# Kernel tuning notes

Measured on AMD Instinct MI355X. Metric: run time of the kernel, lower is better.

Reference implementation:

```python
import jax, jax.numpy as jnp
import numpy as np

B, DIM, NX, NY = 4, 64, 256, 256
HEADS, DIM_HEAD, LATENT, DIM_OUT, KM = 4, 32, 128, 64, 2
DH = DIM_HEAD * KM  # LowRankKernel head dim (also RoPE dim) = 64
EPS = 1e-5
MIN_FREQ = 1.0 / 64.0  # RotaryEmbedding default in FactFormer/LNS repo


def _gelu(x):
    return jax.nn.gelu(x, approximate=False)  # torch nn.GELU default (erf)


def _conv1x1(u, w):
    # u: [b,c,h,w], w: [out,c]  (1x1 conv == channel matmul)
    return jnp.einsum('bchw,oc->bohw', u, w)


def _pooling_reducer(x, win, ln_g, ln_b, w1, w2, b2):
    # x: [b, n_keep, n_pool, c] -> Linear, mean-pool over n_pool, LN+FFN
    h = jnp.einsum('bnmc,hc->bnmh', x, win).mean(axis=2)  # [b, n, hid]
    m = h.mean(axis=-1, keepdims=True)
    v = h.var(axis=-1, keepdims=True)
    h = (h - m) / jnp.sqrt(v + EPS) * ln_g + ln_b
    return _gelu(h @ w1.T) @ w2.T + b2  # [b, n, latent]


def _rope_freqs(n):
    pos = jnp.linspace(0.0, 1.0, n) / MIN_FREQ  # scale/min_freq = 64
    inv = 1.0 / (10000.0 ** (jnp.arange(0, DH, 2, dtype=jnp.float32) / DH))
    f = pos[:, None] * inv[None, :]            # [n, DH//2]
    return jnp.concatenate([f, f], axis=-1)    # [n, DH]


def _apply_rope(x, f):
    # rotate_half = cat(-x2, x1) on half-split (FactFormer convention)
    d = x.shape[-1] // 2
    rot = jnp.concatenate([-x[..., d:], x[..., :d]], axis=-1)
    return x * jnp.cos(f) + rot * jnp.sin(f)


def _low_rank_kernel(x, wqk):
    # x: [b, n, latent] -> K: [b, heads, n, n]; scaling=1, dropout=Identity, qk_norm=False
    b, n, _ = x.shape
    qk = x @ wqk.T
    q, k = jnp.split(qk, 2, axis=-1)
    q = q.reshape(b, n, HEADS, DH).transpose(0, 2, 1, 3)
    k = k.reshape(b, n, HEADS, DH).transpose(0, 2, 1, 3)
    f = _rope_freqs(n)
    q = _apply_rope(q, f)
    k = _apply_rope(k, f)
    return jnp.einsum('bhid,bhjd->bhij', q, k)


def _forward(u, gn_w, gn_b, w_in_proj, w_to_in,
             px_win, px_ln_g, px_ln_b, px_w1, px_w2, px_b2,
             py_win, py_ln_g, py_ln_b, py_w1, py_w2, py_b2,
             kx_wqk, ky_wqk, out_w1, out_w2):
    # GroupNorm(1, dim): normalize over (C,H,W) per sample, affine
    m = u.mean(axis=(1, 2, 3), keepdims=True)
    v = u.var(axis=(1, 2, 3), keepdims=True)
    un = (u - m) / jnp.sqrt(v + EPS) * gn_w[None, :, None, None] + gn_b[None, :, None, None]
    u_phi = _conv1x1(un, w_in_proj)  # [b, heads*dim_head, nx, ny]
    ui = _conv1x1(un, w_to_in)       # [b, dim, nx, ny]
    # to_x: pool over ny -> tokens along nx; to_y: pool over nx -> tokens along ny
    ux = _pooling_reducer(ui.transpose(0, 2, 3, 1), px_win, px_ln_g, px_ln_b, px_w1, px_w2, px_b2)  # [b, nx, latent]
    uy = _pooling_reducer(ui.transpose(0, 3, 2, 1), py_win, py_ln_g, py_ln_b, py_w1, py_w2, py_b2)  # [b, ny, latent]
    kx = _low_rank_kernel(ux, kx_wqk)  # [b, h, nx, nx]
    ky = _low_rank_kernel(uy, ky_wqk)  # [b, h, ny, ny]
    b, hc, nx, ny = u_phi.shape
    up = u_phi.reshape(b, HEADS, hc // HEADS, nx, ny)
    up = jnp.einsum('bhij,bhcjm->bhcim', kx, up)
    up = jnp.einsum('bhlm,bhcim->bhcil', ky, up)
    up = up.reshape(b, hc, nx, ny)
    # InstanceNorm2d (no affine, no running stats)
    m2 = up.mean(axis=(2, 3), keepdims=True)
    v2 = up.var(axis=(2, 3), keepdims=True)
    upn = (up - m2) / jnp.sqrt(v2 + EPS)
    out = _conv1x1(_gelu(_conv1x1(upn, out_w1)), out_w2)
    return out + u


def setup_inputs() -> dict:
    key = jax.random.key(0)
    ks = jax.random.split(key, 16)
    def w(k, shape, s=0.02):
        return (jax.random.normal(k, shape) * s).astype(jnp.float32)
    return {
        'u': jax.random.normal(ks[0], (B, DIM, NX, NY), dtype=jnp.float32),
        'gn_w': jnp.ones((DIM,), jnp.float32), 'gn_b': jnp.zeros((DIM,), jnp.float32),
        'w_in_proj': w(ks[1], (HEADS * DIM_HEAD, DIM)),
        'w_to_in': w(ks[2], (DIM, DIM)),
        'px_win': w(ks[3], (DIM, DIM)),
        'px_ln_g': jnp.ones((DIM,), jnp.float32), 'px_ln_b': jnp.zeros((DIM,), jnp.float32),
        'px_w1': w(ks[4], (2 * DIM, DIM)), 'px_w2': w(ks[5], (LATENT, 2 * DIM)),
        'px_b2': jnp.zeros((LATENT,), jnp.float32),
        'py_win': w(ks[6], (DIM, DIM)),
        'py_ln_g': jnp.ones((DIM,), jnp.float32), 'py_ln_b': jnp.zeros((DIM,), jnp.float32),
        'py_w1': w(ks[7], (2 * DIM, DIM)), 'py_w2': w(ks[8], (LATENT, 2 * DIM)),
        'py_b2': jnp.zeros((LATENT,), jnp.float32),
        'kx_wqk': w(ks[9], (2 * HEADS * DH, LATENT)),
        'ky_wqk': w(ks[10], (2 * HEADS * DH, LATENT)),
        'out_w1': w(ks[11], (DIM_OUT, HEADS * DIM_HEAD)),
        'out_w2': w(ks[12], (DIM_OUT, DIM_OUT)),
    }


def reference(u, gn_w, gn_b, w_in_proj, w_to_in,
              px_win, px_ln_g, px_ln_b, px_w1, px_w2, px_b2,
              py_win, py_ln_g, py_ln_b, py_w1, py_w2, py_b2,
              kx_wqk, ky_wqk, out_w1, out_w2):
    return _forward(u, gn_w, gn_b, w_in_proj, w_to_in,
                    px_win, px_ln_g, px_ln_b, px_w1, px_w2, px_b2,
                    py_win, py_ln_g, py_ln_b, py_w1, py_w2, py_b2,
                    kx_wqk, ky_wqk, out_w1, out_w2)
```

## Files before the change

kernel.cpp:

```cpp
#include <hip/hip_runtime.h>
#include <math.h>

typedef unsigned short ushort_t;
typedef unsigned int uint_t;
typedef __attribute__((ext_vector_type(8))) short s8v;
typedef __attribute__((ext_vector_type(4))) float f4;

#define NPIX 65536
#define EPS_ 1e-5f

__device__ __forceinline__ float bf2f(ushort_t u){ return __uint_as_float(((uint_t)u)<<16); }
__device__ __forceinline__ ushort_t f2bf(float f){
  uint_t u = __float_as_uint(f);
  uint_t r = (u + 0x7fffu + ((u>>16)&1u)) >> 16;
  return (ushort_t)r;
}
__device__ __forceinline__ float bflo(uint_t p){ return __uint_as_float(p<<16); }
__device__ __forceinline__ float bfhi(uint_t p){ return __uint_as_float(p & 0xffff0000u); }
__device__ __forceinline__ uint_t packbf(float a, float b){ return (uint_t)f2bf(a) | ((uint_t)f2bf(b)<<16); }

__device__ __forceinline__ f4 MFMA(s8v a, s8v b, f4 c){
  return __builtin_amdgcn_mfma_f32_16x16x32_bf16(a, b, c, 0, 0, 0);
}

__device__ __forceinline__ float wave_sum(float v){
  #pragma unroll
  for(int m=32;m>=1;m>>=1) v += __shfl_xor(v, m, 64);
  return v;
}

__global__ __launch_bounds__(256) void k1_stats(const float* __restrict__ u,
    float* __restrict__ part, float* __restrict__ pc, float* __restrict__ poolx){
  int blk = blockIdx.x; int b = blk>>8; int c = (blk>>2)&63; int iq = blk&3;
  int t = threadIdx.x; int lane = t&63; int w = t>>6;
  const float* up = u + ((size_t)(b*64+c))*NPIX + iq*64*256;
  __shared__ float sCol[4][256];
  __shared__ float red[8];
  float4 cs4 = {0.f,0.f,0.f,0.f};
  float ss = 0.f;
  #pragma unroll 4
  for(int r16=0;r16<16;r16++){
    int r = w*16 + r16;
    float4 v = *(const float4*)(up + r*256 + lane*4);
    cs4.x+=v.x; cs4.y+=v.y; cs4.z+=v.z; cs4.w+=v.w;
    ss += v.x*v.x+v.y*v.y+v.z*v.z+v.w*v.w;
    float rs = wave_sum(v.x+v.y+v.z+v.w);
    if(lane==0) poolx[(b*256 + iq*64 + r)*64 + c] = rs*(1.f/256.f);
  }
  *(float4*)&sCol[w][lane*4] = cs4;
  float ssw = wave_sum(ss);
  if(lane==0) red[w] = ssw;
  __syncthreads();
  float colsum = sCol[0][t]+sCol[1][t]+sCol[2][t]+sCol[3][t];
  pc[((b*64+c)*4+iq)*256 + t] = colsum;
  float s1 = wave_sum(colsum);
  if(lane==0) red[4+w] = s1;
  __syncthreads();
  if(t==0){
    part[((b*64+c)*4+iq)*2]   = red[4]+red[5]+red[6]+red[7];
    part[((b*64+c)*4+iq)*2+1] = red[0]+red[1]+red[2]+red[3];
  }
}

__global__ void k2_fin(const float* __restrict__ part, float* __restrict__ gnmv){
  int t = threadIdx.x; int b = t>>6; int i = t&63;
  float S1=0.f, S2=0.f;
  #pragma unroll
  for(int q=0;q<4;q++){
    S1 += part[((b*64+i)*4+q)*2];
    S2 += part[((b*64+i)*4+q)*2+1];
  }
  S1 = wave_sum(S1); S2 = wave_sum(S2);
  if(i==0){
    const float inv = 1.f/4194304.f;
    float m = S1*inv; float v = S2*inv - m*m;
    gnmv[b*2] = m; gnmv[b*2+1] = rsqrtf(v + EPS_);
  }
}

__global__ __launch_bounds__(256) void k8a_fold(const float* __restrict__ gnmv,
    const float* __restrict__ gnw, const float* __restrict__ gnb,
    const float* __restrict__ w_in_proj, const float* __restrict__ out_w2,
    ushort_t* __restrict__ wpb, float* __restrict__ c0g, ushort_t* __restrict__ w2b){
  int b = blockIdx.x; int t = threadIdx.x;
  __shared__ float scs[64], shs[64];
  if(t<64){
    float mean = gnmv[b*2], rstd = gnmv[b*2+1];
    float sc = rstd*gnw[t];
    scs[t] = sc; shs[t] = gnb[t] - mean*sc;
  }
  __syncthreads();
  int oc = t>>1, h = t&1;
  float c0 = 0.f;
  for(int k=0;k<32;k++){
    int ch = h*32 + k;
    float wv = w_in_proj[oc*64 + ch];
    wpb[((size_t)b*128 + oc)*64 + ch] = f2bf(wv*scs[ch]);
    c0 += wv*shs[ch];
  }
  c0 += __shfl_xor(c0, 1, 64);
  if(h==0) c0g[b*128 + oc] = c0;
  if(b==0){
    for(int e=t;e<4096;e+=256) w2b[e] = f2bf(out_w2[e]);
  }
}

__global__ void k8b_fold(const float* __restrict__ istat,
    const float* __restrict__ out_w1, ushort_t* __restrict__ W1b,
    float* __restrict__ bias1){
  int b = blockIdx.x; int t = threadIdx.x;
  __shared__ float ms[128], rss[128];
  ms[t] = istat[(b*128+t)*2];       rss[t] = istat[(b*128+t)*2+1];
  ms[64+t] = istat[(b*128+64+t)*2]; rss[64+t] = istat[(b*128+64+t)*2+1];
  __syncthreads();
  float bias = 0.f;
  for(int ch=0;ch<128;ch++){
    float wv = out_w1[t*128 + ch];
    float wr = wv*rss[ch];
    W1b[((size_t)b*64 + t)*128 + ch] = f2bf(wr);
    bias += wr*ms[ch];
  }
  bias1[b*64 + t] = bias;
}

__global__ __launch_bounds__(128) void k3_reduce(
    const float* __restrict__ poolx, const float* __restrict__ pc,
    const float* __restrict__ gnmv,
    const float* __restrict__ gnw, const float* __restrict__ gnb,
    const float* __restrict__ w_to_in,
    const float* __restrict__ xwin, const float* __restrict__ xlg, const float* __restrict__ xlb,
    const float* __restrict__ xw1, const float* __restrict__ xw2, const float* __restrict__ xb2,
    const float* __restrict__ ywin, const float* __restrict__ ylg, const float* __restrict__ ylb,
    const float* __restrict__ yw1, const float* __restrict__ yw2, const float* __restrict__ yb2,
    float* __restrict__ ux, float* __restrict__ uy){
  int id = blockIdx.x;
  int side = id >> 10; int r = id & 1023; int b = r>>8; int i = r&255;
  const float* win = side ? ywin : xwin;
  const float* lg  = side ? ylg  : xlg;
  const float* lb  = side ? ylb  : xlb;
  const float* w1  = side ? yw1  : xw1;
  const float* w2  = side ? yw2  : xw2;
  const float* b2  = side ? yb2  : xb2;
  float* outp = side ? uy : ux;
  int t = threadIdx.x;
  __shared__ float pn[64], t1[64], hh[64], f1[128];
  float mean = gnmv[b*2], rstd = gnmv[b*2+1];
  if(t<64){
    float pv;
    if(side){
      const float* p = pc + ((size_t)(b*64+t)*4)*256 + i;
      pv = (p[0] + p[256] + p[512] + p[768]) * (1.f/256.f);
    } else {
      pv = poolx[(b*256+i)*64 + t];
    }
    pn[t] = (pv - mean)*rstd*gnw[t] + gnb[t];
  }
  __syncthreads();
  if(t<64){
    float acc=0.f; const float* wr = w_to_in + t*64;
    #pragma unroll 8
    for(int c=0;c<64;c++) acc += pn[c]*wr[c];
    t1[t]=acc;
  }
  __syncthreads();
  if(t<64){
    float acc=0.f; const float* wr = win + t*64;
    #pragma unroll 8
    for(int c=0;c<64;c++) acc += t1[c]*wr[c];
    hh[t]=acc;
  }
  __syncthreads();
  if(t<64){
    float v = hh[t];
    float s = wave_sum(v);
    float ss = wave_sum(v*v);
    float m2 = s*(1.f/64.f);
    float var = ss*(1.f/64.f) - m2*m2;
    float rs2 = rsqrtf(var + EPS_);
    hh[t] = (v - m2)*rs2*lg[t] + lb[t];
  }
  __syncthreads();
  {
    float acc=0.f; const float* wr = w1 + t*64;
    #pragma unroll 8
    for(int c=0;c<64;c++) acc += hh[c]*wr[c];
    f1[t] = 0.5f*acc*(1.f + erff(acc*0.70710678118654752f));
  }
  __syncthreads();
  {
    float acc=0.f; const float* wr = w2 + t*128;
    #pragma unroll 8
    for(int j=0;j<128;j++) acc += f1[j]*wr[j];
    outp[(b*256+i)*128 + t] = acc + b2[t];
  }
}

__global__ __launch_bounds__(256) void k4_gemm(
    const float* __restrict__ ux, const float* __restrict__ uy,
    const float* __restrict__ wqkx, const float* __restrict__ wqky,
    ushort_t* __restrict__ qxb, ushort_t* __restrict__ kxTb,
    ushort_t* __restrict__ qyb, ushort_t* __restrict__ kyTb){
  int blk = blockIdx.x;
  int nt = blk&3; int mt = (blk>>2)&1; int b = (blk>>3)&3; int side = blk>>5;
  const float* x  = (side? uy:ux) + (size_t)(b*256 + mt*128)*128;
  const float* wq = (side? wqky:wqkx) + (size_t)nt*128*128;
  ushort_t* qb  = side? qyb : qxb;
  ushort_t* kTb = side? kyTb : kxTb;

  __shared__ __align__(16) ushort_t sA[128*136];
  __shared__ __align__(16) ushort_t sB[128*136];

  int t = threadIdx.x; int lane = t&63; int w = t>>6; int lr = lane&15; int lg = lane>>4;
  for(int e=t;e<4096;e+=256){
    int row = e>>5, c4 = (e&31)*4;
    float4 v = *(const float4*)(x + row*128 + c4);
    uint2 pk; pk.x = packbf(v.x,v.y); pk.y = packbf(v.z,v.w);
    *(uint2*)&sA[row*136 + c4] = pk;
    float4 wv = *(const float4*)(wq + row*128 + c4);
    uint2 wk; wk.x = packbf(wv.x,wv.y); wk.y = packbf(wv.z,wv.w);
    *(uint2*)&sB[row*136 + c4] = wk;
  }
  __syncthreads();
  const f4 fz = {0.f,0.f,0.f,0.f};
  f4 acc[2][8];
  #pragma unroll
  for(int it=0;it<2;it++)
    #pragma unroll
    for(int n2=0;n2<8;n2++) acc[it][n2]=fz;
  #pragma unroll
  for(int kc=0;kc<4;kc++){
    s8v bf[8];
    #pragma unroll
    for(int n2=0;n2<8;n2++)
      bf[n2] = *(const s8v*)&sB[(n2*16+lr)*136 + kc*32 + lg*8];
    #pragma unroll
    for(int it=0;it<2;it++){
      s8v a = *(const s8v*)&sA[(w*32+it*16+lr)*136 + kc*32 + lg*8];
      #pragma unroll
      for(int n2=0;n2<8;n2++)
        acc[it][n2] = MFMA(a, bf[n2], acc[it][n2]);
    }
  }
  if(nt < 2){
    #pragma unroll
    for(int it=0;it<2;it++){
      #pragma unroll
      for(int n2=0;n2<8;n2++){
        int o = nt*128 + n2*16 + lr;
        int h = o>>6, dd = o&63, t32 = dd&31;
        float invf = expf(-(float)t32*(9.210340371976184f/32.f));
        size_t base = (size_t)(b*4+h)*16384;
        #pragma unroll
        for(int r=0;r<4;r++){
          int i = mt*128 + w*32 + it*16 + lg*4 + r;
          float f = (64.f/255.f)*(float)i*invf;
          float sn, cs; __sincosf(f, &sn, &cs);
          float pair = acc[it][n2^2][r];
          float rot = ((n2&2)==0)? -pair : pair;
          float v = acc[it][n2][r]*cs + rot*sn;
          qb[base + (size_t)i*64 + dd] = f2bf(v);
        }
      }
    }
  } else {
    __syncthreads();
    #pragma unroll
    for(int it=0;it<2;it++){
      #pragma unroll
      for(int n2=0;n2<8;n2++){
        int ol = n2*16 + lr;
        int o = nt*128 + ol;
        int t32 = o&31;
        float invf = expf(-(float)t32*(9.210340371976184f/32.f));
        #pragma unroll
        for(int r=0;r<4;r++){
          int il = w*32 + it*16 + lg*4 + r;
          int i = mt*128 + il;
          float f = (64.f/255.f)*(float)i*invf;
          float sn, cs; __sincosf(f, &sn, &cs);
          float pair = acc[it][n2^2][r];
          float rot = ((n2&2)==0)? -pair : pair;
          float v = acc[it][n2][r]*cs + rot*sn;
          sA[ol*136 + il] = f2bf(v);
        }
      }
    }
    __syncthreads();
    {
      int row = t>>1, half = t&1;
      int h = (nt-2)*2 + (row>>6), dd = row&63;
      ushort_t* dst = kTb + (size_t)(b*4+h)*16384 + (size_t)dd*256 + mt*128 + half*64;
      const ushort_t* src = &sA[row*136 + half*64];
      #pragma unroll
      for(int j=0;j<8;j++)
        *(uint4*)(dst + j*8) = *(const uint4*)(src + j*8);
    }
  }
}

__global__ __launch_bounds__(256) void k5s_sums(const ushort_t* __restrict__ kxTb,
    const ushort_t* __restrict__ kyTb, float* __restrict__ ksum){
  int bh = blockIdx.x; int t = threadIdx.x;
  int row = t>>2, g = t&3;
  const ushort_t* kx = kxTb + (size_t)bh*16384 + row*256 + g*64;
  float s = 0.f;
  #pragma unroll
  for(int j=0;j<8;j++){
    uint4 v = *(const uint4*)(kx + j*8);
    s += bflo(v.x)+bfhi(v.x)+bflo(v.y)+bfhi(v.y)+bflo(v.z)+bfhi(v.z)+bflo(v.w)+bfhi(v.w);
  }
  s += __shfl_xor(s,1,64); s += __shfl_xor(s,2,64);
  if(g==0) ksum[bh*128 + row] = s;
  const ushort_t* ky = kyTb + (size_t)bh*16384 + row*256 + g*64;
  float s2 = 0.f;
  #pragma unroll
  for(int j=0;j<8;j++){
    uint4 v = *(const uint4*)(ky + j*8);
    s2 += bflo(v.x)+bfhi(v.x)+bflo(v.y)+bfhi(v.y)+bflo(v.z)+bfhi(v.z)+bflo(v.w)+bfhi(v.w);
  }
  s2 += __shfl_xor(s2,1,64); s2 += __shfl_xor(s2,2,64);
  if(g==0) ksum[bh*128 + 64 + row] = s2;
}

__global__ __launch_bounds__(512) void k7a_core(
    const float* __restrict__ u,
    const ushort_t* __restrict__ kxTb, const ushort_t* __restrict__ kyTb,
    ushort_t* __restrict__ Cb){
  int blk = blockIdx.x; int b = blk>>7; int ch = (blk>>1)&63; int half = blk&1;
  const float* up = u + (size_t)(b*64+ch)*NPIX;
  __shared__ __align__(16) ushort_t su[64*264];
  __shared__ __align__(16) ushort_t sT1[4][64*68];
  int t = threadIdx.x; int w = t>>6; int lane = t&63; int lr = lane&15; int lg = lane>>4;
  int h = w>>1, sub = w&1;
  const ushort_t* KyT = kyTb + (size_t)(b*4+h)*16384;
  const ushort_t* KxT = kxTb + (size_t)(b*4+h)*16384;
  const f4 fz = {0.f,0.f,0.f,0.f};
  f4 cacc[2][4];
  #pragma unroll
  for(int it=0;it<2;it++)
    #pragma unroll
    for(int et=0;et<4;et++) cacc[it][et]=fz;

  for(int jcl=0;jcl<2;jcl++){
    int jc = half*2 + jcl;
    #pragma unroll
    for(int k=0;k<8;k++){
      int flat = k*512 + t;
      int row = flat>>6, col4 = flat&63;
      float4 v = *(const float4*)(up + (size_t)(jc*64+row)*256 + col4*4);
      uint2 pk; pk.x = packbf(v.x,v.y); pk.y = packbf(v.z,v.w);
      *(uint2*)&su[row*264 + col4*4] = pk;
    }
    __syncthreads();
    f4 acc[2][4];
    #pragma unroll
    for(int jt=0;jt<2;jt++)
      #pragma unroll
      for(int et=0;et<4;et++) acc[jt][et]=fz;
    #pragma unroll
    for(int km=0;km<8;km++){
      s8v a0 = *(const s8v*)&su[(sub*32+lr)*264 + km*32 + lg*8];
      s8v a1 = *(const s8v*)&su[(sub*32+16+lr)*264 + km*32 + lg*8];
      #pragma unroll
      for(int et=0;et<4;et++){
        s8v bv = *(const s8v*)(KyT + (et*16+lr)*256 + km*32 + lg*8);
        acc[0][et] = MFMA(a0,bv,acc[0][et]);
        acc[1][et] = MFMA(a1,bv,acc[1][et]);
      }
    }
    #pragma unroll
    for(int jt=0;jt<2;jt++)
      #pragma unroll
      for(int et=0;et<4;et++){
        f4 v = acc[jt][et];
        uint2 pk; pk.x=packbf(v.x,v.y); pk.y=packbf(v.z,v.w);
        *(uint2*)&sT1[h][(et*16+lr)*68 + sub*32 + jt*16 + lg*4] = pk;
      }
    __syncthreads();
    #pragma unroll
    for(int kj=0;kj<2;kj++){
      s8v a0 = *(const s8v*)(KxT + (size_t)(sub*32+lr)*256 + jc*64 + kj*32 + lg*8);
      s8v a1 = *(const s8v*)(KxT + (size_t)(sub*32+16+lr)*256 + jc*64 + kj*32 + lg*8);
      #pragma unroll
      for(int et=0;et<4;et++){
        s8v bv = *(const s8v*)&sT1[h][(et*16+lr)*68 + kj*32 + lg*8];
        cacc[0][et] = MFMA(a0,bv,cacc[0][et]);
        cacc[1][et] = MFMA(a1,bv,cacc[1][et]);
      }
    }
  }
  ushort_t* cbase = Cb + ((size_t)blk*4 + h)*4096;
  #pragma unroll
  for(int it=0;it<2;it++)
    #pragma unroll
    for(int et=0;et<4;et++){
      f4 v = cacc[it][et];
      uint2 pk; pk.x=packbf(v.x,v.y); pk.y=packbf(v.z,v.w);
      *(uint2*)&cbase[(et*16+lr)*64 + sub*32 + it*16 + lg*4] = pk;
    }
}

__global__ __launch_bounds__(256) void k7m_mix(
    const ushort_t* __restrict__ Cb, const ushort_t* __restrict__ wpb,
    const float* __restrict__ c0g, const float* __restrict__ ksum,
    ushort_t* __restrict__ cT){
  int blk = blockIdx.x; int bh = blk>>4; int et = blk&15;
  int b = bh>>2, h = bh&3;
  __shared__ float sWf[32*64];
  __shared__ float sKx[64], sKy4[4];
  int t = threadIdx.x;
  for(int e=t;e<2048;e+=256){
    int ch = e>>6, ic = e&63;
    sWf[e] = bf2f(wpb[((size_t)b*128 + h*32 + ch)*64 + ic]);
  }
  if(t<64) sKx[t] = ksum[bh*128 + t];
  if(t<4)  sKy4[t] = ksum[bh*128 + 64 + et*4 + t];
  __syncthreads();
  int chg = t>>5, edq = t&31, ed0 = edq*8;
  float c0v[4];
  #pragma unroll
  for(int cc=0;cc<4;cc++) c0v[cc] = c0g[b*128 + h*32 + chg*4 + cc];
  float acc[4][8];
  #pragma unroll
  for(int j=0;j<8;j++){
    int ed = ed0 + j;
    float r1 = sKy4[ed>>6]*sKx[ed&63];
    #pragma unroll
    for(int cc=0;cc<4;cc++) acc[cc][j] = c0v[cc]*r1;
  }
  for(int ic=0;ic<64;ic++){
    const ushort_t* p = Cb + ((((size_t)(b*64+ic))*2)*4 + h)*4096 + et*256 + ed0;
    uint4 v0 = *(const uint4*)p;
    uint4 v1 = *(const uint4*)(p + 16384);
    float x[8];
    x[0]=bflo(v0.x)+bflo(v1.x); x[1]=bfhi(v0.x)+bfhi(v1.x);
    x[2]=bflo(v0.y)+bflo(v1.y); x[3]=bfhi(v0.y)+bfhi(v1.y);
    x[4]=bflo(v0.z)+bflo(v1.z); x[5]=bfhi(v0.z)+bfhi(v1.z);
    x[6]=bflo(v0.w)+bflo(v1.w); x[7]=bfhi(v0.w)+bfhi(v1.w);
    #pragma unroll
    for(int cc=0;cc<4;cc++){
      float wv = sWf[(chg*4+cc)*64 + ic];
      #pragma unroll
      for(int j=0;j<8;j++) acc[cc][j] += wv*x[j];
    }
  }
  #pragma unroll
  for(int cc=0;cc<4;cc++){
    uint2 p0, p1;
    p0.x = packbf(acc[cc][0],acc[cc][1]); p0.y = packbf(acc[cc][2],acc[cc][3]);
    p1.x = packbf(acc[cc][4],acc[cc][5]); p1.y = packbf(acc[cc][6],acc[cc][7]);
    ushort_t* dst = cT + ((size_t)bh*32 + chg*4+cc)*4096 + et*256 + ed0;
    *(uint2*)(dst) = p0;
    *(uint2*)(dst+4) = p1;
  }
}

__global__ __launch_bounds__(256) void k7b_heavy(
    const ushort_t* __restrict__ cT,
    const ushort_t* __restrict__ qxb, const ushort_t* __restrict__ qyb,
    ushort_t* __restrict__ up2, float* __restrict__ istat){
  int blk = blockIdx.x;
  int c = blk & 31; int h = (blk>>5)&3; int b = blk>>7;
  int bh = b*4 + h; int ch = h*32 + c;
  const ushort_t* Qx  = qxb + (size_t)bh*16384;
  const ushort_t* Qy  = qyb + (size_t)bh*16384;
  const ushort_t* cTc = cT + (size_t)(bh*32 + c)*4096;
  ushort_t* out_c = up2 + (size_t)(b*128 + ch)*NPIX;

  __shared__ __align__(16) ushort_t sP[256*72];
  __shared__ float sRed[8];

  int t = threadIdx.x; int w = t>>6; int lane = t&63; int lr = lane&15; int lg = lane>>4;
  const f4 fz = {0.f,0.f,0.f,0.f};
  {
    s8v aF[4][2];
    #pragma unroll
    for(int me=0;me<4;me++)
      #pragma unroll
      for(int kd=0;kd<2;kd++)
        aF[me][kd] = *(const s8v*)(cTc + (me*16+lr)*64 + kd*32 + lg*8);
    #pragma unroll
    for(int it=0;it<4;it++){
      s8v b0 = *(const s8v*)(Qx + (w*64+it*16+lr)*64 + lg*8);
      s8v b1 = *(const s8v*)(Qx + (w*64+it*16+lr)*64 + 32 + lg*8);
      #pragma unroll
      for(int me=0;me<4;me++){
        f4 pv = MFMA(aF[me][0], b0, fz);
        pv = MFMA(aF[me][1], b1, pv);
        uint2 pk; pk.x=packbf(pv.x,pv.y); pk.y=packbf(pv.z,pv.w);
        *(uint2*)&sP[(w*64+it*16+lr)*72 + me*16 + lg*4] = pk;
      }
    }
  }
  __syncthreads();
  float lsum=0.f, lssq=0.f;
  {
    s8v aP[4][2];
    #pragma unroll
    for(int it=0;it<4;it++)
      #pragma unroll
      for(int ke=0;ke<2;ke++)
        aP[it][ke] = *(const s8v*)&sP[(w*64+it*16+lr)*72 + ke*32 + lg*8];
    for(int lt=0;lt<4;lt++){
      s8v bq[4][2];
      #pragma unroll
      for(int nt=0;nt<4;nt++)
        #pragma unroll
        for(int ke=0;ke<2;ke++)
          bq[nt][ke] = *(const s8v*)(Qy + (lt*64+nt*16+lr)*64 + ke*32 + lg*8);
      #pragma unroll
      for(int it=0;it<4;it++){
        #pragma unroll
        for(int nt=0;nt<4;nt++){
          f4 o = MFMA(bq[nt][0], aP[it][0], fz);
          o = MFMA(bq[nt][1], aP[it][1], o);
          lsum += o[0]+o[1]+o[2]+o[3];
          lssq += o[0]*o[0]+o[1]*o[1]+o[2]*o[2]+o[3]*o[3];
          uint2 pk; pk.x = packbf(o[0],o[1]); pk.y = packbf(o[2],o[3]);
          *(uint2*)(out_c + (size_t)(w*64 + it*16 + lr)*256 + lt*64 + nt*16 + lg*4) = pk;
        }
      }
    }
  }
  float a1 = wave_sum(lsum), a2 = wave_sum(lssq);
  if(lane==0){ sRed[w]=a1; sRed[4+w]=a2; }
  __syncthreads();
  if(t==0){
    float S = sRed[0]+sRed[1]+sRed[2]+sRed[3];
    float SS = sRed[4]+sRed[5]+sRed[6]+sRed[7];
    float m = S*(1.f/65536.f);
    float var = SS*(1.f/65536.f) - m*m;
    istat[(b*128+ch)*2] = m;
    istat[(b*128+ch)*2+1] = rsqrtf(var + EPS_);
  }
}

__global__ __launch_bounds__(256) void kf_out(
    const ushort_t* __restrict__ up2, const ushort_t* __restrict__ W1b,
    const float* __restrict__ bias1, const ushort_t* __restrict__ w2b,
    const float* __restrict__ u, float* __restrict__ out){
  int blk = blockIdx.x;
  int b = blk>>9; int pix0 = (blk&511)<<7;
  __shared__ __align__(16) unsigned char smraw[128*132*2];
  ushort_t* sX = (ushort_t*)smraw;
  ushort_t* sG = (ushort_t*)smraw;
  float* sO = (float*)smraw;
  int t = threadIdx.x; int lane = t&63; int w = t>>6; int lr = lane&15; int lg = lane>>4;
  {
    int ch = t>>4; int px = (t&15)*8;
    #pragma unroll
    for(int it=0; it<8; it++){
      int c = it*16 + ch;
      uint4 v = *(const uint4*)(up2 + ((size_t)(b*128+c))*NPIX + pix0 + px);
      uint2 lo; lo.x = v.x; lo.y = v.y;
      uint2 hi; hi.x = v.z; hi.y = v.w;
      *(uint2*)&sX[c*132 + px] = lo;
      *(uint2*)&sX[c*132 + px + 4] = hi;
    }
  }
  __syncthreads();
  const ushort_t* w1p = W1b + (size_t)b*64*128;
  f4 g[2][4];
  #pragma unroll
  for(int it=0;it<2;it++)
    #pragma unroll
    for(int nt=0;nt<4;nt++){
      float bv = -bias1[b*64 + nt*16 + lr];
      f4 ci = {bv,bv,bv,bv};
      g[it][nt] = ci;
    }
  #pragma unroll
  for(int kc=0;kc<4;kc++){
    s8v bf[4];
    #pragma unroll
    for(int nt=0;nt<4;nt++)
      bf[nt] = *(const s8v*)(w1p + (nt*16+lr)*128 + kc*32 + lg*8);
    #pragma unroll
    for(int it=0;it<2;it++){
      int pix = w*32 + it*16 + lr;
      s8v a;
      #pragma unroll
      for(int j=0;j<8;j++) a[j] = (short)sX[(kc*32+lg*8+j)*132 + pix];
      #pragma unroll
      for(int nt=0;nt<4;nt++)
        g[it][nt] = MFMA(a, bf[nt], g[it][nt]);
    }
  }
  #pragma unroll
  for(int it=0;it<2;it++)
    #pragma unroll
    for(int nt=0;nt<4;nt++){
      f4 v = g[it][nt];
      #pragma unroll
      for(int r=0;r<4;r++){
        float x = v[r];
        v[r] = 0.5f*x*(1.f + erff(x*0.70710678118654752f));
      }
      g[it][nt] = v;
    }
  __syncthreads();
  #pragma unroll
  for(int it=0;it<2;it++)
    #pragma unroll
    for(int nt=0;nt<4;nt++){
      f4 v = g[it][nt];
      uint2 pk; pk.x = packbf(v.x,v.y); pk.y = packbf(v.z,v.w);
      *(uint2*)&sG[(nt*16+lr)*132 + w*32 + it*16 + lg*4] = pk;
    }
  __syncthreads();
  f4 o2[2][4];
  const f4 fz = {0.f,0.f,0.f,0.f};
  #pragma unroll
  for(int it=0;it<2;it++)
    #pragma unroll
    for(int nt=0;nt<4;nt++) o2[it][nt]=fz;
  #pragma unroll
  for(int kc=0;kc<2;kc++){
    s8v bf[4];
    #pragma unroll
    for(int nt=0;nt<4;nt++)
      bf[nt] = *(const s8v*)(w2b + (nt*16+lr)*64 + kc*32 + lg*8);
    #pragma unroll
    for(int it=0;it<2;it++){
      int pix = w*32 + it*16 + lr;
      s8v a;
      #pragma unroll
      for(int j=0;j<8;j++) a[j] = (short)sG[(kc*32+lg*8+j)*132 + pix];
      #pragma unroll
      for(int nt=0;nt<4;nt++)
        o2[it][nt] = MFMA(a, bf[nt], o2[it][nt]);
    }
  }
  __syncthreads();
  #pragma unroll
  for(int it=0;it<2;it++)
    #pragma unroll
    for(int nt=0;nt<4;nt++)
      *(f4*)&sO[(nt*16+lr)*132 + w*32 + it*16 + lg*4] = o2[it][nt];
  __syncthreads();
  {
    int oc = t>>5; int px = (t&31)*4;
    #pragma unroll
    for(int it=0;it<8;it++){
      int o = it*8 + oc;
      float4 ov = *(const float4*)&sO[o*132 + px];
      float4 uv = *(const float4*)(u + ((size_t)(b*64+o))*NPIX + pix0 + px);
      float4 rv;
      rv.x = ov.x+uv.x; rv.y = ov.y+uv.y; rv.z = ov.z+uv.z; rv.w = ov.w+uv.w;
      *(float4*)(out + ((size_t)(b*64+o))*NPIX + pix0 + px) = rv;
    }
  }
}

extern "C" void kernel_launch(void* const* d_in, const int* in_sizes, int n_in,
                              void* d_out, int out_size, void* d_ws, size_t ws_size,
                              hipStream_t stream) {
  (void)in_sizes; (void)n_in; (void)out_size; (void)ws_size;
  const float* u        = (const float*)d_in[0];
  const float* gnw      = (const float*)d_in[1];
  const float* gnb      = (const float*)d_in[2];
  const float* w_in_proj= (const float*)d_in[3];
  const float* w_to_in  = (const float*)d_in[4];
  const float* px_win   = (const float*)d_in[5];
  const float* px_ln_g  = (const float*)d_in[6];
  const float* px_ln_b  = (const float*)d_in[7];
  const float* px_w1    = (const float*)d_in[8];
  const float* px_w2    = (const float*)d_in[9];
  const float* px_b2    = (const float*)d_in[10];
  const float* py_win   = (const float*)d_in[11];
  const float* py_ln_g  = (const float*)d_in[12];
  const float* py_ln_b  = (const float*)d_in[13];
  const float* py_w1    = (const float*)d_in[14];
  const float* py_w2    = (const float*)d_in[15];
  const float* py_b2    = (const float*)d_in[16];
  const float* kx_wqk   = (const float*)d_in[17];
  const float* ky_wqk   = (const float*)d_in[18];
  const float* out_w1   = (const float*)d_in[19];
  const float* out_w2   = (const float*)d_in[20];
  float* out = (float*)d_out;

  float* fw = (float*)d_ws;
  float* part  = fw + 0;
  float* gnmv  = fw + 2048;
  float* pc    = fw + 4096;
  float* poolx = fw + 266240;
  float* ux    = fw + 397312;
  float* uy    = fw + 528384;
  float* istat = fw + 659456;
  float* c0g   = fw + 660480;
  float* bias1 = fw + 660992;
  ushort_t* wpb = (ushort_t*)(fw + 661504);
  ushort_t* W1b = (ushort_t*)(fw + 677888);
  ushort_t* w2b = (ushort_t*)(fw + 694272);
  float* ksum   = fw + 696320;
  ushort_t* qxb  = (ushort_t*)(fw + 4096);
  ushort_t* kxTb = (ushort_t*)(fw + 135168);
  ushort_t* qyb  = (ushort_t*)(fw + 698368);
  ushort_t* kyTb = (ushort_t*)(fw + 829440);
  ushort_t* up2  = (ushort_t*)(fw + 960512);
  ushort_t* Cb = (ushort_t*)d_out;
  ushort_t* cT = (ushort_t*)d_out + 8388608;

  k1_stats<<<dim3(1024), dim3(256), 0, stream>>>(u, part, pc, poolx);
  k2_fin<<<dim3(1), dim3(256), 0, stream>>>(part, gnmv);
  k8a_fold<<<dim3(4), dim3(256), 0, stream>>>(gnmv, gnw, gnb, w_in_proj, out_w2, wpb, c0g, w2b);
  k3_reduce<<<dim3(2048), dim3(128), 0, stream>>>(poolx, pc, gnmv, gnw, gnb, w_to_in,
      px_win, px_ln_g, px_ln_b, px_w1, px_w2, px_b2,
      py_win, py_ln_g, py_ln_b, py_w1, py_w2, py_b2, ux, uy);
  k4_gemm<<<dim3(64), dim3(256), 0, stream>>>(ux, uy, kx_wqk, ky_wqk, qxb, kxTb, qyb, kyTb);
  k5s_sums<<<dim3(16), dim3(256), 0, stream>>>(kxTb, kyTb, ksum);
  k7a_core<<<dim3(512), dim3(512), 0, stream>>>(u, kxTb, kyTb, Cb);
  k7m_mix<<<dim3(256), dim3(256), 0, stream>>>(Cb, wpb, c0g, ksum, cT);
  k7b_heavy<<<dim3(512), dim3(256), 0, stream>>>(cT, qxb, qyb, up2, istat);
  k8b_fold<<<dim3(4), dim3(64), 0, stream>>>(istat, out_w1, W1b, bias1);
  kf_out<<<dim3(2048), dim3(256), 0, stream>>>(up2, W1b, bias1, w2b, u, out);
}
```

Baseline: 217.8 us.

## Merge k7a half-blocks per channel with double-buffered staging; stage Cb in LDS

k7a_core now runs one block per (batch, channel) instead of two half-blocks, looping over all four 64-row chunks. The next chunk of u is loaded into a second LDS buffer while the current chunk's second GEMM runs. This removes the partial-sum pair that k7m_mix had to add, halving the Cb intermediate and its reads. k7m_mix also stages its Cb tile in LDS with coalesced loads. In exchange k7a launches half as many blocks, which are larger and use more LDS, and it adds an extra barrier per chunk.

```diff
diff --git a/kernel.cpp b/kernel.cpp
--- a/kernel.cpp
+++ b/kernel.cpp
@@ -326,9 +326,9 @@
     const float* __restrict__ u,
     const ushort_t* __restrict__ kxTb, const ushort_t* __restrict__ kyTb,
     ushort_t* __restrict__ Cb){
-  int blk = blockIdx.x; int b = blk>>7; int ch = (blk>>1)&63; int half = blk&1;
-  const float* up = u + (size_t)(b*64+ch)*NPIX;
-  __shared__ __align__(16) ushort_t su[64*264];
+  int blk = blockIdx.x; int b = blk>>6;
+  const float* up = u + (size_t)blk*NPIX;
+  __shared__ __align__(16) ushort_t su[2][64*264];
   __shared__ __align__(16) ushort_t sT1[4][64*68];
   int t = threadIdx.x; int w = t>>6; int lane = t&63; int lr = lane&15; int lg = lane>>4;
   int h = w>>1, sub = w&1;
@@ -341,17 +341,20 @@
     #pragma unroll
     for(int et=0;et<4;et++) cacc[it][et]=fz;
 
-  for(int jcl=0;jcl<2;jcl++){
-    int jc = half*2 + jcl;
+  auto stageld = [&](int jc, int buf){
     #pragma unroll
     for(int k=0;k<8;k++){
       int flat = k*512 + t;
       int row = flat>>6, col4 = flat&63;
       float4 v = *(const float4*)(up + (size_t)(jc*64+row)*256 + col4*4);
       uint2 pk; pk.x = packbf(v.x,v.y); pk.y = packbf(v.z,v.w);
-      *(uint2*)&su[row*264 + col4*4] = pk;
-    }
-    __syncthreads();
+      *(uint2*)&su[buf][row*264 + col4*4] = pk;
+    }
+  };
+  stageld(0, 0);
+  __syncthreads();
+  for(int jc=0;jc<4;jc++){
+    int cur = jc&1;
     f4 acc[2][4];
     #pragma unroll
     for(int jt=0;jt<2;jt++)
@@ -359,8 +362,8 @@
       for(int et=0;et<4;et++) acc[jt][et]=fz;
     #pragma unroll
     for(int km=0;km<8;km++){
-      s8v a0 = *(const s8v*)&su[(sub*32+lr)*264 + km*32 + lg*8];
-      s8v a1 = *(const s8v*)&su[(sub*32+16+lr)*264 + km*32 + lg*8];
+      s8v a0 = *(const s8v*)&su[cur][(sub*32+lr)*264 + km*32 + lg*8];
+      s8v a1 = *(const s8v*)&su[cur][(sub*32+16+lr)*264 + km*32 + lg*8];
       #pragma unroll
       for(int et=0;et<4;et++){
         s8v bv = *(const s8v*)(KyT + (et*16+lr)*256 + km*32 + lg*8);
@@ -377,6 +380,7 @@
         *(uint2*)&sT1[h][(et*16+lr)*68 + sub*32 + jt*16 + lg*4] = pk;
       }
     __syncthreads();
+    if(jc<3) stageld(jc+1, cur^1);
     #pragma unroll
     for(int kj=0;kj<2;kj++){
       s8v a0 = *(const s8v*)(KxT + (size_t)(sub*32+lr)*256 + jc*64 + kj*32 + lg*8);
@@ -388,6 +392,7 @@
         cacc[1][et] = MFMA(a1,bv,cacc[1][et]);
       }
     }
+    __syncthreads();
   }
   ushort_t* cbase = Cb + ((size_t)blk*4 + h)*4096;
   #pragma unroll
@@ -406,9 +411,17 @@
     ushort_t* __restrict__ cT){
   int blk = blockIdx.x; int bh = blk>>4; int et = blk&15;
   int b = bh>>2, h = bh&3;
+  __shared__ __align__(16) ushort_t sC[64*264];
   __shared__ float sWf[32*64];
   __shared__ float sKx[64], sKy4[4];
   int t = threadIdx.x;
+  #pragma unroll
+  for(int k=0;k<8;k++){
+    int flat = k*256 + t;
+    int ic = flat>>5, q = flat&31;
+    uint4 v = *(const uint4*)(Cb + ((size_t)(b*64+ic)*4 + h)*4096 + et*256 + q*8);
+    *(uint4*)&sC[ic*264 + q*8] = v;
+  }
   for(int e=t;e<2048;e+=256){
     int ch = e>>6, ic = e&63;
     sWf[e] = bf2f(wpb[((size_t)b*128 + h*32 + ch)*64 + ic]);
@@ -429,14 +442,10 @@
     for(int cc=0;cc<4;cc++) acc[cc][j] = c0v[cc]*r1;
   }
   for(int ic=0;ic<64;ic++){
-    const ushort_t* p = Cb + ((((size_t)(b*64+ic))*2)*4 + h)*4096 + et*256 + ed0;
-    uint4 v0 = *(const uint4*)p;
-    uint4 v1 = *(const uint4*)(p + 16384);
+    uint4 cv = *(const uint4*)&sC[ic*264 + ed0];
     float x[8];
-    x[0]=bflo(v0.x)+bflo(v1.x); x[1]=bfhi(v0.x)+bfhi(v1.x);
-    x[2]=bflo(v0.y)+bflo(v1.y); x[3]=bfhi(v0.y)+bfhi(v1.y);
-    x[4]=bflo(v0.z)+bflo(v1.z); x[5]=bfhi(v0.z)+bfhi(v1.z);
-    x[6]=bflo(v0.w)+bflo(v1.w); x[7]=bfhi(v0.w)+bfhi(v1.w);
+    x[0]=bflo(cv.x); x[1]=bfhi(cv.x); x[2]=bflo(cv.y); x[3]=bfhi(cv.y);
+    x[4]=bflo(cv.z); x[5]=bfhi(cv.z); x[6]=bflo(cv.w); x[7]=bfhi(cv.w);
     #pragma unroll
     for(int cc=0;cc<4;cc++){
       float wv = sWf[(chg*4+cc)*64 + ic];
@@ -699,7 +708,7 @@
   ushort_t* kyTb = (ushort_t*)(fw + 829440);
   ushort_t* up2  = (ushort_t*)(fw + 960512);
   ushort_t* Cb = (ushort_t*)d_out;
-  ushort_t* cT = (ushort_t*)d_out + 8388608;
+  ushort_t* cT = (ushort_t*)d_out + 4194304;
 
   k1_stats<<<dim3(1024), dim3(256), 0, stream>>>(u, part, pc, poolx);
   k2_fin<<<dim3(1), dim3(256), 0, stream>>>(part, gnmv);
@@ -709,7 +718,7 @@
       py_win, py_ln_g, py_ln_b, py_w1, py_w2, py_b2, ux, uy);
   k4_gemm<<<dim3(64), dim3(256), 0, stream>>>(ux, uy, kx_wqk, ky_wqk, qxb, kxTb, qyb, kyTb);
   k5s_sums<<<dim3(16), dim3(256), 0, stream>>>(kxTb, kyTb, ksum);
-  k7a_core<<<dim3(512), dim3(512), 0, stream>>>(u, kxTb, kyTb, Cb);
+  k7a_core<<<dim3(256), dim3(512), 0, stream>>>(u, kxTb, kyTb, Cb);
   k7m_mix<<<dim3(256), dim3(256), 0, stream>>>(Cb, wpb, c0g, ksum, cT);
   k7b_heavy<<<dim3(512), dim3(256), 0, stream>>>(cT, qxb, qyb, up2, istat);
   k8b_fold<<<dim3(4), dim3(64), 0, stream>>>(istat, out_w1, W1b, bias1);
```

After: 201.1 us. 7.7% less time.
